# Kernel optimization log

Measured on AMD Instinct MI355X. Metric: run time of the kernel, lower is better.

## Reference

```python
import jax, jax.numpy as jnp
import numpy as np

NUM_CLASSES = 256
EMBED_DIM = 1024
PATCH = 16
LN_EPS = 1e-5


def _sincos_pos_2d(hp, wp, dim):
    # Mirrors SemanticMapTokenizer._build_2d_sincos_pos_embed -> [hp, wp, dim]
    d_h = dim // 2
    d_w = dim - d_h
    d_h_even = (d_h // 2) * 2
    d_w_even = (d_w // 2) * 2

    def one_d(length, d_half):
        pos = jnp.arange(length, dtype=jnp.float32)
        omega = 1.0 / (10000.0 ** (jnp.arange(d_half, dtype=jnp.float32) / d_half))
        out = pos[:, None] * omega[None, :]  # [length, d_half]
        return jnp.concatenate([jnp.sin(out), jnp.cos(out)], axis=1)  # [length, 2*d_half]

    emb_h = one_d(hp, d_h_even // 2)  # [hp, d_h_even]
    emb_w = one_d(wp, d_w_even // 2)  # [wp, d_w_even]
    emb_h = jnp.broadcast_to(emb_h[:, None, :], (hp, wp, d_h_even))
    emb_w = jnp.broadcast_to(emb_w[None, :, :], (hp, wp, d_w_even))
    pos = jnp.concatenate([emb_h, emb_w], axis=-1)
    if pos.shape[-1] < dim:
        pos = jnp.concatenate([pos, jnp.zeros((hp, wp, dim - pos.shape[-1]), jnp.float32)], axis=-1)
    elif pos.shape[-1] > dim:
        pos = pos[:, :, :dim]
    return pos


def setup_inputs() -> dict:
    key = jax.random.key(0)
    k1, k2, k3 = jax.random.split(key, 3)
    semantic_map = jax.random.randint(k1, (2, 1, 512, 512), 0, NUM_CLASSES, dtype=jnp.int32)
    embed_table = jax.random.normal(k2, (NUM_CLASSES, EMBED_DIM), dtype=jnp.float32)
    gamma = jnp.ones((EMBED_DIM,), jnp.float32)
    beta = jnp.zeros((EMBED_DIM,), jnp.float32)
    return {"semantic_map": semantic_map, "embed_table": embed_table, "gamma": gamma, "beta": beta}


def reference(semantic_map, embed_table, gamma, beta):
    b, c, h, w = semantic_map.shape
    p = PATCH
    hp, wp = h // p, w // p
    d = embed_table.shape[1]
    # channel 0, round -> clamp -> int index
    idx = jnp.clip(jnp.round(semantic_map[:, 0].astype(jnp.float32)), 0, NUM_CLASSES - 1).astype(jnp.int32)
    pix = embed_table[idx]  # [B, H, W, D] -- large intermediate (gather)
    # AvgPool2d(kernel=stride=p): mean over non-overlapping p x p patches
    pooled = pix[:, : hp * p, : wp * p, :].reshape(b, hp, p, wp, p, d).mean(axis=(2, 4))  # [B, hp, wp, D]
    pooled = pooled + _sincos_pos_2d(hp, wp, d)[None]
    tokens = pooled.reshape(b, hp * wp, d)
    # LayerNorm over last dim
    mu = tokens.mean(axis=-1, keepdims=True)
    var = jnp.mean(jnp.square(tokens - mu), axis=-1, keepdims=True)
    tokens = (tokens - mu) * jax.lax.rsqrt(var + LN_EPS) * gamma + beta
    return tokens
```

## Files before the change

kernel.cpp:

```cpp
#include <hip/hip_runtime.h>

#define IMG   512
#define NCLS  256
#define DIM   1024
#define HPW   32
#define TPB   8
#define NT2   1024

typedef short bf16x8 __attribute__((ext_vector_type(8)));
typedef float f32x4  __attribute__((ext_vector_type(4)));

__device__ inline ushort bf16rne(float v) {
    unsigned u = __float_as_uint(v);
    return (ushort)((u + 0x7fffu + ((u >> 16) & 1u)) >> 16);
}

__global__ __launch_bounds__(256)
void prep(const int* __restrict__ smap, const float* __restrict__ table,
          ushort* __restrict__ Tt2, ushort* __restrict__ Ab)
{
    __shared__ ushort   tile[16][264];
    __shared__ unsigned cnt[TPB * NCLS];
    const int t   = threadIdx.x;
    const int bid = blockIdx.x;

    if (bid < 64) {
        const int dtile = bid;
        const int d0    = dtile * 16;
        {
            const float* src = table + (size_t)t * DIM + d0;
            #pragma unroll
            for (int q = 0; q < 4; ++q) {
                const float4 v = *reinterpret_cast<const float4*>(src + q * 4);
                tile[q * 4 + 0][t] = bf16rne(v.x);
                tile[q * 4 + 1][t] = bf16rne(v.y);
                tile[q * 4 + 2][t] = bf16rne(v.z);
                tile[q * 4 + 3][t] = bf16rne(v.w);
            }
        }
        __syncthreads();
        const int ks   = t >> 5;
        const int g    = (t >> 3) & 3;
        const int c0   = (t & 7) * 2;
        const int cls0 = ks * 32 + g * 8;
        uint4* dst = reinterpret_cast<uint4*>(Tt2 + (size_t)dtile * 4096 + (size_t)t * 16);
        dst[0] = *reinterpret_cast<const uint4*>(&tile[c0][cls0]);
        dst[1] = *reinterpret_cast<const uint4*>(&tile[c0 + 1][cls0]);
    } else {
        const int grp  = bid - 64;
        const int tok0 = grp * TPB;
        const int b    = tok0 >> 10;
        const int ph   = (tok0 >> 5) & 31;
        const int pw0  = tok0 & 31;

        #pragma unroll
        for (int i = t; i < TPB * NCLS; i += 256) cnt[i] = 0u;
        __syncthreads();

        {
            const int row = t >> 4;
            const int col = (t & 15) * 8;
            const int* bp = smap + ((size_t)b * IMG + (size_t)(ph * 16 + row)) * IMG
                                 + pw0 * 16 + col;
            const int4 q0 = *reinterpret_cast<const int4*>(bp);
            const int4 q1 = *reinterpret_cast<const int4*>(bp + 4);
            unsigned* hp = &cnt[(col >> 4) * NCLS];
            atomicAdd(&hp[min(max(q0.x, 0), NCLS - 1)], 1u);
            atomicAdd(&hp[min(max(q0.y, 0), NCLS - 1)], 1u);
            atomicAdd(&hp[min(max(q0.z, 0), NCLS - 1)], 1u);
            atomicAdd(&hp[min(max(q0.w, 0), NCLS - 1)], 1u);
            atomicAdd(&hp[min(max(q1.x, 0), NCLS - 1)], 1u);
            atomicAdd(&hp[min(max(q1.y, 0), NCLS - 1)], 1u);
            atomicAdd(&hp[min(max(q1.z, 0), NCLS - 1)], 1u);
            atomicAdd(&hp[min(max(q1.w, 0), NCLS - 1)], 1u);
        }
        __syncthreads();

        ushort* ab = Ab + (size_t)grp * 4096;
        #pragma unroll
        for (int i = t; i < 4096; i += 256) {
            ushort v = 0;
            if (i < TPB * NCLS)
                v = (ushort)(__float_as_uint((float)cnt[i] * (1.f / 256.f)) >> 16);
            ab[i] = v;
        }
    }
}

__global__ __launch_bounds__(NT2)
void gemm_ln(const ushort* __restrict__ Ab, const ushort* __restrict__ Tt2,
             const float* __restrict__ gamma, const float* __restrict__ beta,
             float* __restrict__ out)
{
    __shared__ ushort cntb[16][264];
    __shared__ float  red[16][2][4][2];

    const int t    = threadIdx.x;
    const int lane = t & 63;
    const int w    = t >> 6;
    const int c    = lane & 15;
    const int g    = lane >> 4;

    const int tok0 = blockIdx.x * TPB;
    const int ph   = (tok0 >> 5) & 31;
    const int pw0  = tok0 & 31;

    {
        const ushort4 v = reinterpret_cast<const ushort4*>(Ab + (size_t)blockIdx.x * 4096)[t];
        const int idx = t * 4;
        *reinterpret_cast<ushort4*>(&cntb[idx >> 8][idx & 255]) = v;
    }
    __syncthreads();

    f32x4 acc[4];
    #pragma unroll
    for (int i = 0; i < 4; ++i) acc[i] = (f32x4){0.f, 0.f, 0.f, 0.f};

    const ushort* bt = Tt2 + (size_t)(w * 4) * 4096 + (size_t)lane * 8;
    #pragma unroll 2
    for (int ks = 0; ks < 8; ++ks) {
        const bf16x8 a = *reinterpret_cast<const bf16x8*>(&cntb[c][ks * 32 + g * 8]);
        bf16x8 bfv[4];
        #pragma unroll
        for (int nf = 0; nf < 4; ++nf)
            bfv[nf] = *reinterpret_cast<const bf16x8*>(bt + (size_t)nf * 4096 + ks * 512);
        #pragma unroll
        for (int nf = 0; nf < 4; ++nf)
            acc[nf] = __builtin_amdgcn_mfma_f32_16x16x32_bf16(a, bfv[nf], acc[nf], 0, 0, 0);
    }

    const int quad   = w >> 2;
    const int cosSel = quad & 1;
    float ls[4]  = {0, 0, 0, 0};
    float ls2[4] = {0, 0, 0, 0};

    #pragma unroll
    for (int nf = 0; nf < 4; ++nf) {
        const int dlow = (w & 3) * 64 + nf * 16 + c;
        const float omega = exp2f((float)dlow * (-13.287712379549449f / 256.f));
        if (quad < 2) {
            float sv, cv; __sincosf((float)ph * omega, &sv, &cv);
            const float v = cosSel ? cv : sv;
            #pragma unroll
            for (int i = 0; i < 4; ++i) acc[nf][i] += v;
        } else {
            #pragma unroll
            for (int i = 0; i < 4; ++i) {
                float sv, cv; __sincosf((float)(pw0 + g * 4 + i) * omega, &sv, &cv);
                acc[nf][i] += cosSel ? cv : sv;
            }
        }
        #pragma unroll
        for (int i = 0; i < 4; ++i) { ls[i] += acc[nf][i]; ls2[i] += acc[nf][i] * acc[nf][i]; }
    }

    #pragma unroll
    for (int off = 1; off < 16; off <<= 1) {
        #pragma unroll
        for (int i = 0; i < 4; ++i) {
            ls[i]  += __shfl_xor(ls[i],  off, 64);
            ls2[i] += __shfl_xor(ls2[i], off, 64);
        }
    }
    if (c == 0 && g < 2) {
        #pragma unroll
        for (int i = 0; i < 4; ++i) { red[w][g][i][0] = ls[i]; red[w][g][i][1] = ls2[i]; }
    }
    __syncthreads();

    if (g < 2) {
        float mu[4], rs[4];
        #pragma unroll
        for (int i = 0; i < 4; ++i) {
            float S = 0.f, S2 = 0.f;
            #pragma unroll
            for (int ww = 0; ww < 16; ++ww) { S += red[ww][g][i][0]; S2 += red[ww][g][i][1]; }
            mu[i] = S * (1.f / DIM);
            rs[i] = rsqrtf(S2 * (1.f / DIM) - mu[i] * mu[i] + 1e-5f);
        }
        #pragma unroll
        for (int nf = 0; nf < 4; ++nf) {
            const int d = w * 64 + nf * 16 + c;
            const float gv = gamma[d], bv = beta[d];
            #pragma unroll
            for (int i = 0; i < 4; ++i) {
                const int r = g * 4 + i;
                out[(size_t)(tok0 + r) * DIM + d] = (acc[nf][i] - mu[i]) * rs[i] * gv + bv;
            }
        }
    }
}

extern "C" void kernel_launch(void* const* d_in, const int* in_sizes, int n_in,
                              void* d_out, int out_size, void* d_ws, size_t ws_size,
                              hipStream_t stream) {
    const int*   smap  = (const int*)d_in[0];
    const float* table = (const float*)d_in[1];
    const float* gamma = (const float*)d_in[2];
    const float* beta  = (const float*)d_in[3];
    float*       out   = (float*)d_out;

    const int batches = in_sizes[0] / (IMG * IMG);
    const int tokens  = batches * HPW * HPW;
    const int ngrp    = tokens / TPB;

    ushort* Tt2 = (ushort*)d_ws;
    ushort* Ab  = Tt2 + (size_t)64 * 4096;

    prep<<<64 + ngrp, 256, 0, stream>>>(smap, table, Tt2, Ab);
    gemm_ln<<<ngrp, NT2, 0, stream>>>(Ab, Tt2, gamma, beta, out);
}
```

Before: 21.87 us.

## Process 16 tokens per block to fill all MFMA rows

Raises tokens per block from 8 to 16 so the 16-row MFMA A-tile holds real tokens instead of zero padding. The count is 2048 tokens, so this halves the number of histogram and GEMM blocks and halves redundant B-matrix loads per token. Each histogram thread now scans one full patch row of 16 pixels, and all four lane groups take part in the LayerNorm reduction and the output store. The cost is fewer blocks, 128 GEMM blocks for a 256-CU device, which lowers parallelism and may leave CUs idle.

```diff
diff --git a/kernel.cpp b/kernel.cpp
--- a/kernel.cpp
+++ b/kernel.cpp
@@ -4,7 +4,7 @@
 #define NCLS  256
 #define DIM   1024
 #define HPW   32
-#define TPB   8
+#define TPB   16
 #define NT2   1024
 
 typedef short bf16x8 __attribute__((ext_vector_type(8)));
@@ -59,31 +59,25 @@
 
         {
             const int row = t >> 4;
-            const int col = (t & 15) * 8;
+            const int p   = t & 15;
             const int* bp = smap + ((size_t)b * IMG + (size_t)(ph * 16 + row)) * IMG
-                                 + pw0 * 16 + col;
-            const int4 q0 = *reinterpret_cast<const int4*>(bp);
-            const int4 q1 = *reinterpret_cast<const int4*>(bp + 4);
-            unsigned* hp = &cnt[(col >> 4) * NCLS];
-            atomicAdd(&hp[min(max(q0.x, 0), NCLS - 1)], 1u);
-            atomicAdd(&hp[min(max(q0.y, 0), NCLS - 1)], 1u);
-            atomicAdd(&hp[min(max(q0.z, 0), NCLS - 1)], 1u);
-            atomicAdd(&hp[min(max(q0.w, 0), NCLS - 1)], 1u);
-            atomicAdd(&hp[min(max(q1.x, 0), NCLS - 1)], 1u);
-            atomicAdd(&hp[min(max(q1.y, 0), NCLS - 1)], 1u);
-            atomicAdd(&hp[min(max(q1.z, 0), NCLS - 1)], 1u);
-            atomicAdd(&hp[min(max(q1.w, 0), NCLS - 1)], 1u);
+                                 + (pw0 + p) * 16;
+            unsigned* hp = &cnt[p * NCLS];
+            #pragma unroll
+            for (int q4 = 0; q4 < 4; ++q4) {
+                const int4 q = *reinterpret_cast<const int4*>(bp + q4 * 4);
+                atomicAdd(&hp[min(max(q.x, 0), NCLS - 1)], 1u);
+                atomicAdd(&hp[min(max(q.y, 0), NCLS - 1)], 1u);
+                atomicAdd(&hp[min(max(q.z, 0), NCLS - 1)], 1u);
+                atomicAdd(&hp[min(max(q.w, 0), NCLS - 1)], 1u);
+            }
         }
         __syncthreads();
 
         ushort* ab = Ab + (size_t)grp * 4096;
         #pragma unroll
-        for (int i = t; i < 4096; i += 256) {
-            ushort v = 0;
-            if (i < TPB * NCLS)
-                v = (ushort)(__float_as_uint((float)cnt[i] * (1.f / 256.f)) >> 16);
-            ab[i] = v;
-        }
+        for (int i = t; i < TPB * NCLS; i += 256)
+            ab[i] = (ushort)(__float_as_uint((float)cnt[i] * (1.f / 256.f)) >> 16);
     }
 }
 
@@ -93,7 +87,7 @@
              float* __restrict__ out)
 {
     __shared__ ushort cntb[16][264];
-    __shared__ float  red[16][2][4][2];
+    __shared__ float  red[16][4][4][2];
 
     const int t    = threadIdx.x;
     const int lane = t & 63;
@@ -162,13 +156,13 @@
             ls2[i] += __shfl_xor(ls2[i], off, 64);
         }
     }
-    if (c == 0 && g < 2) {
+    if (c == 0) {
         #pragma unroll
         for (int i = 0; i < 4; ++i) { red[w][g][i][0] = ls[i]; red[w][g][i][1] = ls2[i]; }
     }
     __syncthreads();
 
-    if (g < 2) {
+    {
         float mu[4], rs[4];
         #pragma unroll
         for (int i = 0; i < 4; ++i) {
```

Result: faster. 19.97 us (median of 2 runs) (-8.7%).
